# Optimization experiments

Hardware: AMD Instinct MI355X
Metric: run time of the kernel (lower is better)

Reference implementation:

```python
import jax, jax.numpy as jnp
import numpy as np
import math

B, T, C, NH = 8, 1024, 768, 12
HD = C // NH
EPS = 1e-5

def layer_norm(x, g, b):
    mu = jnp.mean(x, axis=-1, keepdims=True)
    var = jnp.mean(jnp.square(x - mu), axis=-1, keepdims=True)
    return (x - mu) * jax.lax.rsqrt(var + EPS) * g + b

def setup_inputs() -> dict:
    key = jax.random.key(0)
    ks = jax.random.split(key, 10)
    s = lambda n: 1.0 / math.sqrt(n)
    return {
        "x": jax.random.normal(ks[0], (B, T, C), jnp.float32),
        "attn_mask": jax.random.randint(ks[1], (B, T), 0, 2, jnp.int32),
        "ln1_g": jnp.ones((C,), jnp.float32),
        "ln1_b": jnp.zeros((C,), jnp.float32),
        "W_attn": jax.random.normal(ks[2], (C, 3 * C), jnp.float32) * s(C),
        "b_attn": jnp.zeros((3 * C,), jnp.float32),
        "W_proj": jax.random.normal(ks[3], (C, C), jnp.float32) * s(C),
        "b_proj": jnp.zeros((C,), jnp.float32),
        "ln2_g": jnp.ones((C,), jnp.float32),
        "ln2_b": jnp.zeros((C,), jnp.float32),
        "W_fc": jax.random.normal(ks[4], (C, 4 * C), jnp.float32) * s(C),
        "b_fc": jnp.zeros((4 * C,), jnp.float32),
        "W_fc2": jax.random.normal(ks[5], (4 * C, C), jnp.float32) * s(4 * C),
        "b_fc2": jnp.zeros((C,), jnp.float32),
    }

def reference(x, attn_mask, ln1_g, ln1_b, W_attn, b_attn, W_proj, b_proj,
              ln2_g, ln2_b, W_fc, b_fc, W_fc2, b_fc2):
    # --- attention branch ---
    h = layer_norm(x, ln1_g, ln1_b)                     # [B,T,C]
    qkv = h @ W_attn + b_attn                           # [B,T,3C]
    q, k, v = jnp.split(qkv, 3, axis=-1)
    q = q.reshape(B, T, NH, HD).transpose(0, 2, 1, 3)   # [B,H,T,D]
    k = k.reshape(B, T, NH, HD).transpose(0, 2, 1, 3)
    v = v.reshape(B, T, NH, HD).transpose(0, 2, 1, 3)
    attn = jnp.einsum('bhqd,bhkd->bhqk', q, k) * (1.0 / math.sqrt(HD))
    mask = attn_mask[:, None, None, :]                  # [B,1,1,T] key-padding
    attn = jnp.where(mask == 0, -jnp.inf, attn)
    attn = jax.nn.softmax(attn, axis=-1)
    o = jnp.einsum('bhqk,bhkd->bhqd', attn, v)          # [B,H,T,D]
    o = o.transpose(0, 2, 1, 3).reshape(B, T, C)
    x = x + (o @ W_proj + b_proj)
    # --- MLP branch ---
    h2 = layer_norm(x, ln2_g, ln2_b)
    h2 = jax.nn.gelu(h2 @ W_fc + b_fc, approximate=True)
    x = x + (h2 @ W_fc2 + b_fc2)
    return x
```

## Files before the change

### kernel.cpp

```cpp
#include <hip/hip_runtime.h>
#include <hip/hip_bf16.h>
#include <math.h>

constexpr int kB  = 8;
constexpr int kT  = 1024;
constexpr int kC  = 768;
constexpr int kNH = 12;
constexpr int kHD = 64;
constexpr int kM  = kB * kT;
constexpr int k3C = 3 * kC;
constexpr int k4C = 4 * kC;

typedef __bf16 bf16x8 __attribute__((ext_vector_type(8)));
typedef float  f32x4  __attribute__((ext_vector_type(4)));
typedef unsigned short u16x8 __attribute__((ext_vector_type(8)));

__device__ inline void gload_lds16(const void* g, void* l) {
  __builtin_amdgcn_global_load_lds(
      (const __attribute__((address_space(1))) void*)g,
      (__attribute__((address_space(3))) void*)l, 16, 0, 0);
}

__global__ __launch_bounds__(256) void ln_kernel(
    const float* __restrict__ x, const float* __restrict__ g,
    const float* __restrict__ bta, __hip_bfloat16* __restrict__ out)
{
  __shared__ float red[4];
  int row = blockIdx.x;
  int tid = threadIdx.x;
  const float* xr = x + (size_t)row * kC;
  float v0 = xr[tid], v1 = xr[tid + 256], v2 = xr[tid + 512];

  float s = v0 + v1 + v2;
#pragma unroll
  for (int off = 32; off; off >>= 1) s += __shfl_xor(s, off);
  if ((tid & 63) == 0) red[tid >> 6] = s;
  __syncthreads();
  float mu = (red[0] + red[1] + red[2] + red[3]) * (1.0f / kC);

  float d0 = v0 - mu, d1 = v1 - mu, d2 = v2 - mu;
  float q = d0 * d0 + d1 * d1 + d2 * d2;
#pragma unroll
  for (int off = 32; off; off >>= 1) q += __shfl_xor(q, off);
  __syncthreads();
  if ((tid & 63) == 0) red[tid >> 6] = q;
  __syncthreads();
  float var = (red[0] + red[1] + red[2] + red[3]) * (1.0f / kC);
  float inv = rsqrtf(var + 1e-5f);

  __hip_bfloat16* orow = out + (size_t)row * kC;
  orow[tid]       = __float2bfloat16(d0 * inv * g[tid]       + bta[tid]);
  orow[tid + 256] = __float2bfloat16(d1 * inv * g[tid + 256] + bta[tid + 256]);
  orow[tid + 512] = __float2bfloat16(d2 * inv * g[tid + 512] + bta[tid + 512]);
}

__global__ __launch_bounds__(256) void transpose_cast(
    const float* __restrict__ W, __hip_bfloat16* __restrict__ WT, int K, int N)
{
  __shared__ __hip_bfloat16 t[64][65];
  int k0 = blockIdx.y * 64, n0 = blockIdx.x * 64;
  int tid = threadIdx.x;
#pragma unroll
  for (int it = 0; it < 16; ++it) {
    int e = it * 256 + tid;
    int r = e >> 6, c = e & 63;
    t[r][c] = __float2bfloat16(W[(size_t)(k0 + r) * N + n0 + c]);
  }
  __syncthreads();
#pragma unroll
  for (int it = 0; it < 16; ++it) {
    int e = it * 256 + tid;
    int nr = e >> 6, kc = e & 63;
    WT[(size_t)(n0 + nr) * K + k0 + kc] = t[kc][nr];
  }
}

__global__ __launch_bounds__(256) void v_transpose(
    const __hip_bfloat16* __restrict__ qkv, __hip_bfloat16* __restrict__ vt)
{
  __shared__ __hip_bfloat16 tile[64][80];
  int b = blockIdx.z, h = blockIdx.y, t0 = blockIdx.x * 64;
  int tid = threadIdx.x;
  const __hip_bfloat16* vb = qkv + (size_t)(b * kT) * k3C + 2 * kC + h * kHD;
#pragma unroll
  for (int it = 0; it < 2; ++it) {
    int e = it * 256 + tid;
    int r = e >> 3, c8 = (e & 7) * 8;
    *(u16x8*)&tile[r][c8] = *(const u16x8*)(vb + (size_t)(t0 + r) * k3C + c8);
  }
  __syncthreads();
  __hip_bfloat16* vrow = vt + (size_t)(b * kNH + h) * kHD * kT;
#pragma unroll
  for (int it = 0; it < 2; ++it) {
    int e = it * 256 + tid;
    int d = e >> 3, k8 = (e & 7) * 8;
    u16x8 u;
#pragma unroll
    for (int m = 0; m < 8; ++m)
      u[m] = *(const unsigned short*)&tile[k8 + m][d];
    *(u16x8*)(vrow + (size_t)d * kT + t0 + k8) = u;
  }
}

__device__ inline float gelu_tanh(float c) {
  float t = 0.7978845608028654f * (c + 0.044715f * c * c * c);
  return 0.5f * c * (1.0f + tanhf(t));
}

template <int OUT_MODE>
__global__ __launch_bounds__(256) void gemm_bf16(
    const __hip_bfloat16* __restrict__ A,
    const __hip_bfloat16* __restrict__ WT,
    const float* __restrict__ bias,
    const float* __restrict__ R,
    void* __restrict__ outv, int M, int N, int K)
{
  __shared__ __align__(16) __hip_bfloat16 sh[2][2][128 * 64];
  const int tid  = threadIdx.x;
  const int lane = tid & 63, wid = tid >> 6;
  const int wr = wid >> 1, wc = wid & 1;
  const int r16 = lane & 15, g = lane >> 4;

  const int nwg = gridDim.x * gridDim.y;
  const int bid = blockIdx.y * gridDim.x + blockIdx.x;
  const int swz = (bid & 7) * (nwg >> 3) + (bid >> 3);
  const int m0 = (swz / gridDim.x) * 128;
  const int n0 = (swz % gridDim.x) * 128;

  const __hip_bfloat16* Abase = A  + (size_t)m0 * K;
  const __hip_bfloat16* Bbase = WT + (size_t)n0 * K;

  f32x4 acc[4][4] = {};

  auto stage = [&](int t) {
    const int buf = t & 1;
    const __hip_bfloat16* As = Abase + t * 64;
    const __hip_bfloat16* Bs = Bbase + t * 64;
#pragma unroll
    for (int it = 0; it < 4; ++it) {
      int e = it * 256 + tid;
      int row = e >> 3, ch = (e & 7) ^ (row & 7);
      char* la = (char*)&sh[buf][0][0] + (it * 4096 + (tid & ~63) * 16);
      char* lb = (char*)&sh[buf][1][0] + (it * 4096 + (tid & ~63) * 16);
      gload_lds16(As + (size_t)row * K + ch * 8, la);
      gload_lds16(Bs + (size_t)row * K + ch * 8, lb);
    }
  };

  const int NT = K >> 6;
  stage(0);
  __syncthreads();

  for (int t = 0; t < NT; ++t) {
    const int buf = t & 1;
    if (t + 1 < NT) stage(t + 1);
    const char* Ab = (const char*)&sh[buf][0][0];
    const char* Bb = (const char*)&sh[buf][1][0];
#pragma unroll
    for (int s = 0; s < 2; ++s) {
      bf16x8 af[4], bf[4];
#pragma unroll
      for (int i = 0; i < 4; ++i) {
        int ar = wr * 64 + i * 16 + r16;
        af[i] = *(const bf16x8*)(Ab + ar * 128 + (((s * 4 + g) ^ (ar & 7)) << 4));
        int br = wc * 64 + i * 16 + r16;
        bf[i] = *(const bf16x8*)(Bb + br * 128 + (((s * 4 + g) ^ (br & 7)) << 4));
      }
#pragma unroll
      for (int i = 0; i < 4; ++i)
#pragma unroll
        for (int j = 0; j < 4; ++j)
          acc[i][j] = __builtin_amdgcn_mfma_f32_16x16x32_bf16(af[i], bf[j],
                                                              acc[i][j], 0, 0, 0);
    }
    __syncthreads();
  }

  const int r0 = m0 + wr * 64 + g * 4;
  const int c0 = n0 + wc * 64 + r16;
#pragma unroll
  for (int i = 0; i < 4; ++i) {
#pragma unroll
    for (int j = 0; j < 4; ++j) {
      int col = c0 + j * 16;
      float bv = bias[col];
#pragma unroll
      for (int q = 0; q < 4; ++q) {
        int row = r0 + i * 16 + q;
        float c = acc[i][j][q] + bv;
        if (OUT_MODE == 1) {
          c += R[(size_t)row * N + col];
          ((float*)outv)[(size_t)row * N + col] = c;
        } else {
          if (OUT_MODE == 2) c = gelu_tanh(c);
          ((__hip_bfloat16*)outv)[(size_t)row * N + col] = __float2bfloat16(c);
        }
      }
    }
  }
}

__global__ __launch_bounds__(256) void attn_mfma(
    const __hip_bfloat16* __restrict__ qkv,
    const __hip_bfloat16* __restrict__ vt,
    const int* __restrict__ mask,
    __hip_bfloat16* __restrict__ o)
{
  __shared__ __align__(16) __hip_bfloat16 Ks[64 * 64];
  __shared__ __align__(16) __hip_bfloat16 Vs[64 * 64];
  __shared__ __align__(16) __hip_bfloat16 Ps[4 * 16 * 64];

  const int b = blockIdx.z, h = blockIdx.y, q0 = blockIdx.x * 64;
  const int tid = threadIdx.x, lane = tid & 63, wid = tid >> 6;
  const int r16 = lane & 15, g = lane >> 4;
  const size_t rs = k3C;
  const __hip_bfloat16* qb = qkv + (size_t)(b * kT) * rs + h * kHD;
  const __hip_bfloat16* kb = qb + kC;
  const __hip_bfloat16* vtb = vt + (size_t)(b * kNH + h) * kHD * kT;
  const int* mrow = mask + b * kT;
  constexpr float kSc = 0.125f * 1.4426950408889634f;

  bf16x8 qf[2];
  {
    const __hip_bfloat16* qr = qb + (size_t)(q0 + wid * 16 + r16) * rs;
#pragma unroll
    for (int s = 0; s < 2; ++s) qf[s] = *(const bf16x8*)(qr + s * 32 + g * 8);
  }

  f32x4 o_acc[4] = {};
  float l_part[4] = {0.f, 0.f, 0.f, 0.f};

  __hip_bfloat16* Pw = Ps + wid * 1024;

  for (int t = 0; t < 16; ++t) {
    __syncthreads();
#pragma unroll
    for (int it = 0; it < 2; ++it) {
      int e = it * 256 + tid;
      int row = e >> 3, ch = (e & 7) ^ (row & 7);
      char* lk = (char*)Ks + (it * 4096 + (tid & ~63) * 16);
      char* lv = (char*)Vs + (it * 4096 + (tid & ~63) * 16);
      gload_lds16(kb + (size_t)(t * 64 + row) * rs + ch * 8, lk);
      gload_lds16(vtb + (size_t)row * kT + t * 64 + ch * 8, lv);
    }
    __syncthreads();

    f32x4 sa[4] = {};
#pragma unroll
    for (int j = 0; j < 4; ++j) {
#pragma unroll
      for (int s = 0; s < 2; ++s) {
        int kr = 16 * j + r16;
        bf16x8 kf = *(const bf16x8*)((const char*)Ks + kr * 128 +
                                     (((s * 4 + g) ^ (kr & 7)) << 4));
        sa[j] = __builtin_amdgcn_mfma_f32_16x16x32_bf16(qf[s], kf, sa[j], 0, 0, 0);
      }
    }

    float keep[4];
#pragma unroll
    for (int j = 0; j < 4; ++j)
      keep[j] = (mrow[t * 64 + 16 * j + r16] != 0) ? 1.f : 0.f;

#pragma unroll
    for (int r = 0; r < 4; ++r) {
      float p[4];
#pragma unroll
      for (int j = 0; j < 4; ++j)
        p[j] = keep[j] != 0.f ? exp2f(sa[j][r] * kSc) : 0.f;
      l_part[r] += (p[0] + p[1]) + (p[2] + p[3]);
      int q = g * 4 + r;
      char* pwq = (char*)Pw + q * 128 + (r16 & 7) * 2;
#pragma unroll
      for (int j = 0; j < 4; ++j) {
        int chn = ((j << 1) | (r16 >> 3)) ^ (q & 7);
        *(__hip_bfloat16*)(pwq + (chn << 4)) = __float2bfloat16(p[j]);
      }
    }

    asm volatile("s_waitcnt lgkmcnt(0)" ::: "memory");
    __builtin_amdgcn_sched_barrier(0);

#pragma unroll
    for (int s = 0; s < 2; ++s) {
      bf16x8 pf = *(const bf16x8*)((const char*)Pw + r16 * 128 +
                                   (((s * 4 + g) ^ (r16 & 7)) << 4));
#pragma unroll
      for (int db = 0; db < 4; ++db) {
        int vr = 16 * db + r16;
        bf16x8 vf = *(const bf16x8*)((const char*)Vs + vr * 128 +
                                     (((s * 4 + g) ^ (vr & 7)) << 4));
        o_acc[db] = __builtin_amdgcn_mfma_f32_16x16x32_bf16(pf, vf, o_acc[db], 0, 0, 0);
      }
    }
  }

#pragma unroll
  for (int r = 0; r < 4; ++r) {
    float l = l_part[r];
#pragma unroll
    for (int off = 8; off; off >>= 1) l += __shfl_xor(l, off);
    float inv = 1.f / l;
    size_t row = (size_t)(b * kT) + q0 + wid * 16 + g * 4 + r;
#pragma unroll
    for (int db = 0; db < 4; ++db)
      o[row * kC + h * kHD + 16 * db + r16] = __float2bfloat16(o_acc[db][r] * inv);
  }
}

extern "C" void kernel_launch(void* const* d_in, const int* in_sizes, int n_in,
                              void* d_out, int out_size, void* d_ws, size_t ws_size,
                              hipStream_t stream) {
  const float* x      = (const float*)d_in[0];
  const int*   amask  = (const int*)  d_in[1];
  const float* ln1_g  = (const float*)d_in[2];
  const float* ln1_b  = (const float*)d_in[3];
  const float* W_attn = (const float*)d_in[4];
  const float* b_attn = (const float*)d_in[5];
  const float* W_proj = (const float*)d_in[6];
  const float* b_proj = (const float*)d_in[7];
  const float* ln2_g  = (const float*)d_in[8];
  const float* ln2_b  = (const float*)d_in[9];
  const float* W_fc   = (const float*)d_in[10];
  const float* b_fc   = (const float*)d_in[11];
  const float* W_fc2  = (const float*)d_in[12];
  const float* b_fc2  = (const float*)d_in[13];
  float* out = (float*)d_out;

  char* ws = (char*)d_ws;
  __hip_bfloat16* h_bf    = (__hip_bfloat16*)(ws);
  __hip_bfloat16* qkv_bf  = (__hip_bfloat16*)(ws + (size_t)16 * 1024 * 1024);
  __hip_bfloat16* fc_bf   = qkv_bf;
  __hip_bfloat16* wt_attn = (__hip_bfloat16*)(ws + (size_t)68 * 1024 * 1024);
  __hip_bfloat16* wt_proj = (__hip_bfloat16*)(ws + (size_t)72 * 1024 * 1024);
  __hip_bfloat16* wt_fc   = (__hip_bfloat16*)(ws + (size_t)74 * 1024 * 1024);
  __hip_bfloat16* wt_fc2  = (__hip_bfloat16*)(ws + (size_t)79 * 1024 * 1024);
  __hip_bfloat16* vt_bf   = (__hip_bfloat16*)(ws + (size_t)84 * 1024 * 1024);

  dim3 blk(256);

  transpose_cast<<<dim3(k3C / 64, kC / 64), blk, 0, stream>>>(W_attn, wt_attn, kC, k3C);
  transpose_cast<<<dim3(kC / 64, kC / 64), blk, 0, stream>>>(W_proj, wt_proj, kC, kC);
  transpose_cast<<<dim3(k4C / 64, kC / 64), blk, 0, stream>>>(W_fc, wt_fc, kC, k4C);
  transpose_cast<<<dim3(kC / 64, k4C / 64), blk, 0, stream>>>(W_fc2, wt_fc2, k4C, kC);

  ln_kernel<<<kM, blk, 0, stream>>>(x, ln1_g, ln1_b, h_bf);
  gemm_bf16<0><<<dim3(k3C / 128, kM / 128), blk, 0, stream>>>(
      h_bf, wt_attn, b_attn, nullptr, qkv_bf, kM, k3C, kC);
  v_transpose<<<dim3(kT / 64, kNH, kB), blk, 0, stream>>>(qkv_bf, vt_bf);
  attn_mfma<<<dim3(kT / 64, kNH, kB), blk, 0, stream>>>(qkv_bf, vt_bf, amask, h_bf);
  gemm_bf16<1><<<dim3(kC / 128, kM / 128), blk, 0, stream>>>(
      h_bf, wt_proj, b_proj, x, out, kM, kC, kC);
  ln_kernel<<<kM, blk, 0, stream>>>(out, ln2_g, ln2_b, h_bf);
  gemm_bf16<2><<<dim3(k4C / 128, kM / 128), blk, 0, stream>>>(
      h_bf, wt_fc, b_fc, nullptr, fc_bf, kM, k4C, kC);
  gemm_bf16<1><<<dim3(kC / 128, kM / 128), blk, 0, stream>>>(
      fc_bf, wt_fc2, b_fc2, out, out, kM, kC, k4C);
}
```

Measured before the change: 267.1 us.

## Store residual intermediate in bf16, unroll GEMM double buffer, fast GELU

The post-attention residual is now written as bf16 into a reused workspace buffer instead of fp32, so the second layernorm and the final GEMM read half the bytes. The GEMM main loop is unrolled by two with fixed ping-pong buffers, which removes dynamic buffer indexing. GELU's tanhf is replaced by an exp2/rcp formulation. The trade-off is reduced precision in the residual stream and a slightly less accurate GELU, and the unrolled loop assumes K/64 is even.

```diff
diff --git a/kernel.cpp b/kernel.cpp
--- a/kernel.cpp
+++ b/kernel.cpp
@@ -21,15 +21,19 @@
       (__attribute__((address_space(3))) void*)l, 16, 0, 0);
 }
 
+__device__ inline float ldx(const float* p) { return *p; }
+__device__ inline float ldx(const __hip_bfloat16* p) { return __bfloat162float(*p); }
+
+template <typename TIN>
 __global__ __launch_bounds__(256) void ln_kernel(
-    const float* __restrict__ x, const float* __restrict__ g,
+    const TIN* __restrict__ x, const float* __restrict__ g,
     const float* __restrict__ bta, __hip_bfloat16* __restrict__ out)
 {
   __shared__ float red[4];
   int row = blockIdx.x;
   int tid = threadIdx.x;
-  const float* xr = x + (size_t)row * kC;
-  float v0 = xr[tid], v1 = xr[tid + 256], v2 = xr[tid + 512];
+  const TIN* xr = x + (size_t)row * kC;
+  float v0 = ldx(xr + tid), v1 = ldx(xr + tid + 256), v2 = ldx(xr + tid + 512);
 
   float s = v0 + v1 + v2;
 #pragma unroll
@@ -102,20 +106,23 @@
   }
 }
 
-__device__ inline float gelu_tanh(float c) {
+__device__ inline float gelu_fast(float c) {
   float t = 0.7978845608028654f * (c + 0.044715f * c * c * c);
-  return 0.5f * c * (1.0f + tanhf(t));
-}
-
-template <int OUT_MODE>
+  float e = exp2f(t * 2.8853900817779268f);
+  float th = 1.0f - 2.0f * __builtin_amdgcn_rcpf(e + 1.0f);
+  return 0.5f * c * (1.0f + th);
+}
+
+template <int MODE>
 __global__ __launch_bounds__(256) void gemm_bf16(
     const __hip_bfloat16* __restrict__ A,
     const __hip_bfloat16* __restrict__ WT,
     const float* __restrict__ bias,
-    const float* __restrict__ R,
+    const void* __restrict__ Rv,
     void* __restrict__ outv, int M, int N, int K)
 {
-  __shared__ __align__(16) __hip_bfloat16 sh[2][2][128 * 64];
+  __shared__ __align__(16) __hip_bfloat16 As[2][128 * 64];
+  __shared__ __align__(16) __hip_bfloat16 Bs[2][128 * 64];
   const int tid  = threadIdx.x;
   const int lane = tid & 63, wid = tid >> 6;
   const int wr = wid >> 1, wc = wid & 1;
@@ -132,30 +139,21 @@
 
   f32x4 acc[4][4] = {};
 
-  auto stage = [&](int t) {
-    const int buf = t & 1;
-    const __hip_bfloat16* As = Abase + t * 64;
-    const __hip_bfloat16* Bs = Bbase + t * 64;
+  auto stage = [&](int t, int buf) {
+    const __hip_bfloat16* Ap = Abase + t * 64;
+    const __hip_bfloat16* Bp = Bbase + t * 64;
 #pragma unroll
     for (int it = 0; it < 4; ++it) {
       int e = it * 256 + tid;
       int row = e >> 3, ch = (e & 7) ^ (row & 7);
-      char* la = (char*)&sh[buf][0][0] + (it * 4096 + (tid & ~63) * 16);
-      char* lb = (char*)&sh[buf][1][0] + (it * 4096 + (tid & ~63) * 16);
-      gload_lds16(As + (size_t)row * K + ch * 8, la);
-      gload_lds16(Bs + (size_t)row * K + ch * 8, lb);
+      char* la = (char*)&As[buf][0] + (it * 4096 + (tid & ~63) * 16);
+      char* lb = (char*)&Bs[buf][0] + (it * 4096 + (tid & ~63) * 16);
+      gload_lds16(Ap + (size_t)row * K + ch * 8, la);
+      gload_lds16(Bp + (size_t)row * K + ch * 8, lb);
     }
   };
 
-  const int NT = K >> 6;
-  stage(0);
-  __syncthreads();
-
-  for (int t = 0; t < NT; ++t) {
-    const int buf = t & 1;
-    if (t + 1 < NT) stage(t + 1);
-    const char* Ab = (const char*)&sh[buf][0][0];
-    const char* Bb = (const char*)&sh[buf][1][0];
+  auto compute = [&](const char* Ab, const char* Bb) {
 #pragma unroll
     for (int s = 0; s < 2; ++s) {
       bf16x8 af[4], bf[4];
@@ -173,6 +171,18 @@
           acc[i][j] = __builtin_amdgcn_mfma_f32_16x16x32_bf16(af[i], bf[j],
                                                               acc[i][j], 0, 0, 0);
     }
+  };
+
+  const int NT = K >> 6;
+  stage(0, 0);
+  __syncthreads();
+
+  for (int t = 0; t < NT; t += 2) {
+    stage(t + 1, 1);
+    compute((const char*)&As[0][0], (const char*)&Bs[0][0]);
+    __syncthreads();
+    if (t + 2 < NT) stage(t + 2, 0);
+    compute((const char*)&As[1][0], (const char*)&Bs[1][0]);
     __syncthreads();
   }
 
@@ -188,11 +198,14 @@
       for (int q = 0; q < 4; ++q) {
         int row = r0 + i * 16 + q;
         float c = acc[i][j][q] + bv;
-        if (OUT_MODE == 1) {
-          c += R[(size_t)row * N + col];
+        if (MODE == 3) {
+          c += ((const float*)Rv)[(size_t)row * N + col];
+          ((__hip_bfloat16*)outv)[(size_t)row * N + col] = __float2bfloat16(c);
+        } else if (MODE == 4) {
+          c += __bfloat162float(((const __hip_bfloat16*)Rv)[(size_t)row * N + col]);
           ((float*)outv)[(size_t)row * N + col] = c;
         } else {
-          if (OUT_MODE == 2) c = gelu_tanh(c);
+          if (MODE == 2) c = gelu_fast(c);
           ((__hip_bfloat16*)outv)[(size_t)row * N + col] = __float2bfloat16(c);
         }
       }
@@ -336,6 +349,7 @@
   __hip_bfloat16* wt_fc   = (__hip_bfloat16*)(ws + (size_t)74 * 1024 * 1024);
   __hip_bfloat16* wt_fc2  = (__hip_bfloat16*)(ws + (size_t)79 * 1024 * 1024);
   __hip_bfloat16* vt_bf   = (__hip_bfloat16*)(ws + (size_t)84 * 1024 * 1024);
+  __hip_bfloat16* x1_bf   = vt_bf;
 
   dim3 blk(256);
 
@@ -344,16 +358,16 @@
   transpose_cast<<<dim3(k4C / 64, kC / 64), blk, 0, stream>>>(W_fc, wt_fc, kC, k4C);
   transpose_cast<<<dim3(kC / 64, k4C / 64), blk, 0, stream>>>(W_fc2, wt_fc2, k4C, kC);
 
-  ln_kernel<<<kM, blk, 0, stream>>>(x, ln1_g, ln1_b, h_bf);
+  ln_kernel<float><<<kM, blk, 0, stream>>>(x, ln1_g, ln1_b, h_bf);
   gemm_bf16<0><<<dim3(k3C / 128, kM / 128), blk, 0, stream>>>(
       h_bf, wt_attn, b_attn, nullptr, qkv_bf, kM, k3C, kC);
   v_transpose<<<dim3(kT / 64, kNH, kB), blk, 0, stream>>>(qkv_bf, vt_bf);
   attn_mfma<<<dim3(kT / 64, kNH, kB), blk, 0, stream>>>(qkv_bf, vt_bf, amask, h_bf);
-  gemm_bf16<1><<<dim3(kC / 128, kM / 128), blk, 0, stream>>>(
-      h_bf, wt_proj, b_proj, x, out, kM, kC, kC);
-  ln_kernel<<<kM, blk, 0, stream>>>(out, ln2_g, ln2_b, h_bf);
+  gemm_bf16<3><<<dim3(kC / 128, kM / 128), blk, 0, stream>>>(
+      h_bf, wt_proj, b_proj, x, x1_bf, kM, kC, kC);
+  ln_kernel<__hip_bfloat16><<<kM, blk, 0, stream>>>(x1_bf, ln2_g, ln2_b, h_bf);
   gemm_bf16<2><<<dim3(k4C / 128, kM / 128), blk, 0, stream>>>(
       h_bf, wt_fc, b_fc, nullptr, fc_bf, kM, k4C, kC);
-  gemm_bf16<1><<<dim3(kC / 128, kM / 128), blk, 0, stream>>>(
-      fc_bf, wt_fc2, b_fc2, out, out, kM, kC, k4C);
-}
+  gemm_bf16<4><<<dim3(kC / 128, kM / 128), blk, 0, stream>>>(
+      fc_bf, wt_fc2, b_fc2, x1_bf, out, kM, kC, k4C);
+}
```

After: 285.7 us. 1.07x slower.
